# Optimization experiments

Hardware: AMD Instinct MI355X
Metric: run time of the kernel (lower is better)

## Reference

```python
import jax, jax.numpy as jnp
import numpy as np

N = 1024      # params.input_dim (f1 is a square [N, N] similarity matrix)
TOPK = 16     # params.topk
B = 64        # hardcoded batch in the original reshape
W = 2 * N // B  # spatial width after reshape


def setup_inputs() -> dict:
    key = jax.random.key(0)
    k1, k2, k3 = jax.random.split(key, 3)
    f1 = jax.random.normal(k1, (N, N), dtype=jnp.float32)
    # Conv2d(in=N, out=N, kernel=(TOPK, 1)) weights, kaiming-ish scale
    conv_w = jax.random.normal(k2, (N, N, TOPK, 1), dtype=jnp.float32) * 0.01
    conv_b = jax.random.normal(k3, (N,), dtype=jnp.float32) * 0.01
    return {"f1": f1, "conv_w": conv_w, "conv_b": conv_b}


def reference(f1, conv_w, conv_b):
    # i = topk indices along last dim (largest, sorted) -> [N, TOPK]
    _, idx = jax.lax.top_k(f1, TOPK)
    # pos = f1[i]: gather rows of f1 by the topk column indices -> [N, TOPK, N]
    pos = f1[idx]
    # repeat_interleave(TOPK, dim=0).reshape(N, TOPK, -1) == each row tiled TOPK times
    rep = jnp.broadcast_to(f1[:, None, :], (N, TOPK, N))
    # cat on dim=2 -> [N, TOPK, 2N]; reshape to NCHW [B, N, TOPK, W]
    out = jnp.concatenate([rep, pos], axis=2).reshape(B, N, TOPK, W)
    # Conv2d kernel (TOPK, 1), VALID padding collapses H -> 1: [B, N, 1, W]
    y = jax.lax.conv_general_dilated(
        out, conv_w, window_strides=(1, 1), padding='VALID',
        dimension_numbers=('NCHW', 'OIHW', 'NCHW'))
    y = y + conv_b[None, :, None, None]
    return jax.nn.relu(y).reshape(N, -1)  # [N, B*W] = [N, 2N]
```

## Files before the change

### kernel.cpp

```cpp
#include <hip/hip_runtime.h>
#include <stdint.h>


#define NDIM 1024
#define TK   16
#define KPOS 8192
#define KREP 512
#define NCOL 2048

typedef unsigned short u16;
typedef uint32_t u32;
typedef u16   u16x8  __attribute__((ext_vector_type(8)));
typedef __bf16 bf16x8 __attribute__((ext_vector_type(8)));
typedef float  f32x4  __attribute__((ext_vector_type(4)));

__device__ __forceinline__ u16 f2bf(float x) {
    union { float f; unsigned u; } v; v.f = x;
    unsigned r = 0x7FFFu + ((v.u >> 16) & 1u);
    return (u16)((v.u + r) >> 16);
}

__device__ __forceinline__ void load_lds_16B(const u16* g, u16* l) {
    __builtin_amdgcn_global_load_lds(
        (__attribute__((address_space(1))) void*)(uintptr_t)g,
        (__attribute__((address_space(3))) void*)(unsigned)(uintptr_t)l,
        16, 0, 0);
}

#define PREP_TOPK 256
#define PREP_ZERO 512
#define PREP_W    1024
#define PREP_F1T  256

__global__ __launch_bounds__(256) void prep_kernel(const float* __restrict__ f1,
                                                   const float* __restrict__ W,
                                                   int* __restrict__ idx,
                                                   u16* __restrict__ Wb,
                                                   u16* __restrict__ W1b,
                                                   u16* __restrict__ f1t,
                                                   float* __restrict__ out) {
    const int bid = blockIdx.x;
    const int t = threadIdx.x;
    if (bid < PREP_TOPK) {
        const int lane = t & 63;
        const int row  = bid * 4 + (t >> 6);
        float v[16];
        const float* src = f1 + row * NDIM + lane;
        #pragma unroll
        for (int j = 0; j < 16; ++j) v[j] = src[j * 64];
        for (int sel = 0; sel < TK; ++sel) {
            float best = -3.402823466e38f; int bg = 0x7fffffff;
            #pragma unroll
            for (int j = 0; j < 16; ++j)
                if (v[j] > best) { best = v[j]; bg = j * 64 + lane; }
            #pragma unroll
            for (int s = 1; s < 64; s <<= 1) {
                float ov = __shfl_xor(best, s);
                int   og = __shfl_xor(bg, s);
                if (ov > best || (ov == best && og < bg)) { best = ov; bg = og; }
            }
            if (lane == sel) idx[row * TK + sel] = bg;
            #pragma unroll
            for (int j = 0; j < 16; ++j)
                if (bg == j * 64 + lane) v[j] = -3.402823466e38f;
        }
    } else if (bid < PREP_TOPK + PREP_ZERO) {
        const int zb = bid - PREP_TOPK;
        f32x4 z = {0.f, 0.f, 0.f, 0.f};
        float* p = out + (size_t)zb * 4096 + t * 16;
        #pragma unroll
        for (int j = 0; j < 4; ++j) *(f32x4*)(p + j * 4) = z;
    } else if (bid < PREP_TOPK + PREP_ZERO + PREP_W) {
        const int o = bid - PREP_TOPK - PREP_ZERO;
        const float* wrow = W + (size_t)o * 16384;
        u16* wbrow = Wb + (size_t)o * KPOS;
        #pragma unroll
        for (int j = 0; j < 4; ++j) {
            const int v = j * 2048 + t * 8;
            const int u = ((v >> 5) << 6) + 32 + (v & 31);
            float4 a = *(const float4*)(wrow + u);
            float4 b = *(const float4*)(wrow + u + 4);
            u16x8 ov;
            ov[0] = f2bf(a.x); ov[1] = f2bf(a.y); ov[2] = f2bf(a.z); ov[3] = f2bf(a.w);
            ov[4] = f2bf(b.x); ov[5] = f2bf(b.y); ov[6] = f2bf(b.z); ov[7] = f2bf(b.w);
            *(u16x8*)(wbrow + v) = ov;
        }
        #pragma unroll
        for (int h = 0; h < 2; ++h) {
            const int kr = h * 256 + t;
            const int nl = kr >> 5, e = kr & 31;
            const float* base = wrow + nl * 1024 + e;
            float s = 0.f;
            #pragma unroll
            for (int tt = 0; tt < 16; ++tt) s += base[tt * 64];
            W1b[o * KREP + kr] = f2bf(s);
        }
    } else {
        const int gb = bid - PREP_TOPK - PREP_ZERO - PREP_W;
        const int unit = t >> 5;
        const int w = t & 31;
        const int rq = gb * 8 + unit;
        const int row = rq >> 1, q = rq & 1;
        const float* src = f1 + row * NDIM + q * 512;
        const int swp = ((w >> 2) & 1) * 8;
        u16 tmp[16];
        #pragma unroll
        for (int kh = 0; kh < 16; ++kh)
            tmp[kh ^ swp] = f2bf(src[kh * 32 + w]);
        u16* dst = f1t + ((size_t)row * 2 + q) * 512 + w * 16;
        *(u16x8*)(dst)     = *(u16x8*)(tmp);
        *(u16x8*)(dst + 8) = *(u16x8*)(tmp + 8);
    }
}

#define BM 128
#define BN 128
#define BK 64
#define KITERS 34

__global__ __launch_bounds__(256, 2) void gemm_kernel(const u16* __restrict__ Ap,
                                                      const u16* __restrict__ A1,
                                                      const u16* __restrict__ f1t,
                                                      const int* __restrict__ idx,
                                                      float* __restrict__ out) {
    __shared__ __align__(16) u16 As[2][BM * BK];
    __shared__ __align__(16) u16 Bs[2][16 * 512];
    __shared__ int idxL[256];
    const int f = blockIdx.x;
    const int m = f & 7;
    const int g = f >> 3;
    const int n = g & 15;
    const int z = g >> 4;
    const int t    = threadIdx.x;
    const int lane = t & 63;
    const int wave = t >> 6;
    const int wm   = (wave >> 1) * 64;
    const int wn   = (wave & 1) * 64;
    const int quad = lane >> 4;
    const int l16  = lane & 15;
    const int sw   = l16 & 7;
    const int o0 = m * BM;
    const int n0 = n * BN;
    const int nb0 = n * 4;
    const int kb = z * 2048;
    const int nl0 = z * 4;

    {
        const int bl = t >> 6, nlz = (t >> 4) & 3, tt = t & 15;
        idxL[t] = idx[((nb0 + bl) * 16 + nl0 + nlz) * TK + tt];
    }

    f32x4 acc[4][4] = {};

    const int rA = t >> 3;
    const int c8 = t & 7;
    const int csw = (c8 ^ (rA & 7)) * 8;
    const u16* gApos = Ap + (size_t)(o0 + rA) * KPOS + kb + csw;
    const u16* gArep = A1 + (size_t)(o0 + rA) * KREP + z * 128 + csw;
    const int ipbp = kb >> 4;
    const int ipbr = z * 8;

    auto stage = [&](int it, int nb) {
        u16* lA = As[nb] + t * 8;
        int rows[4], qp;
        if (it < 32) {
            const int k0 = it * BK;
            #pragma unroll
            for (int c = 0; c < 4; ++c)
                load_lds_16B(gApos + (size_t)(c * 32) * KPOS + k0, lA + c * 2048);
            const int ip = ipbp + it * 4 + wave;
            qp = ip & 1;
            const int nlz = (ip >> 5) & 3, tt = (ip >> 1) & 15;
            #pragma unroll
            for (int bl = 0; bl < 4; ++bl)
                rows[bl] = idxL[bl * 64 + nlz * 16 + tt];
        } else {
            const int k0 = (it - 32) * BK;
            #pragma unroll
            for (int c = 0; c < 4; ++c)
                load_lds_16B(gArep + (size_t)(c * 32) * KREP + k0, lA + c * 2048);
            const int ip = ipbr + (it - 32) * 4 + wave;
            qp = ip & 1;
            const int nlr = ip >> 1;
            #pragma unroll
            for (int bl = 0; bl < 4; ++bl)
                rows[bl] = (nb0 + bl) * 16 + nlr;
        }
        #pragma unroll
        for (int bl = 0; bl < 4; ++bl)
            load_lds_16B(f1t + ((size_t)rows[bl] * 2 + qp) * 512 + lane * 8,
                         Bs[nb] + (wave * 4 + bl) * 512);
    };

    __syncthreads();
    stage(0, 0);
    __syncthreads();

    for (int it = 0; it < KITERS; ++it) {
        const int cur = it & 1;
        if (it + 1 < KITERS) stage(it + 1, 1 - cur);

        #pragma unroll
        for (int ks = 0; ks < 2; ++ks) {
            bf16x8 af[4], bfr[4];
            #pragma unroll
            for (int mt = 0; mt < 4; ++mt) {
                u16x8 bits = *(const u16x8*)(As[cur] + (wm + mt * 16 + l16) * BK
                                                + (((ks * 4 + quad) ^ sw) * 8));
                af[mt] = __builtin_bit_cast(bf16x8, bits);
            }
            const int ci2 = ks * 2 + (quad >> 1);
            const int qh  = quad & 1;
            #pragma unroll
            for (int nt = 0; nt < 4; ++nt) {
                const int nn = wn + nt * 16 + l16;
                const int blocf = nn >> 5, w = nn & 31;
                u16x8 bits = *(const u16x8*)(Bs[cur] + (ci2 * 4 + blocf) * 512 + w * 16
                                                + ((qh ^ ((w >> 2) & 1)) * 8));
                bfr[nt] = __builtin_bit_cast(bf16x8, bits);
            }
            #pragma unroll
            for (int mt = 0; mt < 4; ++mt)
                #pragma unroll
                for (int nt = 0; nt < 4; ++nt)
                    acc[mt][nt] = __builtin_amdgcn_mfma_f32_16x16x32_bf16(
                        af[mt], bfr[nt], acc[mt][nt], 0, 0, 0);
        }
        __syncthreads();
    }

    #pragma unroll
    for (int nt = 0; nt < 4; ++nt) {
        const int nn = n0 + wn + nt * 16 + l16;
        const int bb = nn >> 5, w = nn & 31;
        #pragma unroll
        for (int mt = 0; mt < 4; ++mt) {
            #pragma unroll
            for (int r = 0; r < 4; ++r) {
                const int o = o0 + wm + mt * 16 + quad * 4 + r;
                unsafeAtomicAdd(out + (size_t)(bb * 16 + (o >> 6)) * 2048
                                    + (o & 63) * 32 + w,
                                acc[mt][nt][r]);
            }
        }
    }
}

__global__ __launch_bounds__(256) void finalize_kernel(float* __restrict__ out,
                                                       const float* __restrict__ bias) {
    const int tid = blockIdx.x * 256 + threadIdx.x;
    const int f = tid * 4;
    const int o = ((f >> 11) & 15) * 64 + ((f & 2047) >> 5);
    const float bv = bias[o];
    float4 x = *(float4*)(out + f);
    x.x = fmaxf(x.x + bv, 0.f);
    x.y = fmaxf(x.y + bv, 0.f);
    x.z = fmaxf(x.z + bv, 0.f);
    x.w = fmaxf(x.w + bv, 0.f);
    *(float4*)(out + f) = x;
}

extern "C" void kernel_launch(void* const* d_in, const int* in_sizes, int n_in,
                              void* d_out, int out_size, void* d_ws, size_t ws_size,
                              hipStream_t stream) {
    const float* f1   = (const float*)d_in[0];
    const float* Wc   = (const float*)d_in[1];
    const float* bias = (const float*)d_in[2];
    float* out = (float*)d_out;

    int* idx = (int*)d_ws;
    u16* Wb  = (u16*)((char*)d_ws + 65536);
    u16* W1b = (u16*)((char*)d_ws + 16842752);
    u16* f1t = (u16*)((char*)d_ws + 17891328);

    prep_kernel<<<PREP_TOPK + PREP_ZERO + PREP_W + PREP_F1T,
                  256, 0, stream>>>(f1, Wc, idx, Wb, W1b, f1t, out);
    gemm_kernel<<<512, 256, 0, stream>>>(Wb, W1b, f1t, idx, out);
    finalize_kernel<<<(NDIM * NCOL) / (4 * 256), 256, 0, stream>>>(out, bias);
}
```

Before: 164.1 us.

## Halve GEMM K-tile and double split-K blocks for higher occupancy

Cuts the GEMM K step from 64 to 32 and doubles the split-K factor, so 1024 blocks are launched instead of 512 and each block covers half the K range. LDS use per block is halved and launch bounds now request 4 blocks per CU, which is meant to raise occupancy and spread work more evenly across CUs. The staging index math, LDS swizzle and idx preload are reworked to match. In exchange, twice as many float atomic adds go to the output, and each iteration has fewer MFMAs per barrier, which may add synchronisation overhead.

```diff
diff --git a/kernel.cpp b/kernel.cpp
--- a/kernel.cpp
+++ b/kernel.cpp
@@ -115,17 +115,17 @@
 
 #define BM 128
 #define BN 128
-#define BK 64
+#define BK 32
 #define KITERS 34
 
-__global__ __launch_bounds__(256, 2) void gemm_kernel(const u16* __restrict__ Ap,
+__global__ __launch_bounds__(256, 4) void gemm_kernel(const u16* __restrict__ Ap,
                                                       const u16* __restrict__ A1,
                                                       const u16* __restrict__ f1t,
                                                       const int* __restrict__ idx,
                                                       float* __restrict__ out) {
     __shared__ __align__(16) u16 As[2][BM * BK];
-    __shared__ __align__(16) u16 Bs[2][16 * 512];
-    __shared__ int idxL[256];
+    __shared__ __align__(16) u16 Bs[2][8 * 512];
+    __shared__ int idxL[128];
     const int f = blockIdx.x;
     const int m = f & 7;
     const int g = f >> 3;
@@ -138,58 +138,49 @@
     const int wn   = (wave & 1) * 64;
     const int quad = lane >> 4;
     const int l16  = lane & 15;
-    const int sw   = l16 & 7;
+    const int key16 = (l16 >> 1) & 3;
     const int o0 = m * BM;
     const int n0 = n * BN;
     const int nb0 = n * 4;
-    const int kb = z * 2048;
-    const int nl0 = z * 4;
-
-    {
-        const int bl = t >> 6, nlz = (t >> 4) & 3, tt = t & 15;
-        idxL[t] = idx[((nb0 + bl) * 16 + nl0 + nlz) * TK + tt];
+    const int kb = z * 1024;
+
+    if (t < 128) {
+        const int bl = t >> 5, nlz = (t >> 4) & 1, tt = t & 15;
+        idxL[t] = idx[((nb0 + bl) * 16 + z * 2 + nlz) * TK + tt];
     }
 
     f32x4 acc[4][4] = {};
 
-    const int rA = t >> 3;
-    const int c8 = t & 7;
-    const int csw = (c8 ^ (rA & 7)) * 8;
+    const int rA = t >> 2;
+    const int csw = ((t & 3) ^ ((t >> 3) & 3)) * 8;
     const u16* gApos = Ap + (size_t)(o0 + rA) * KPOS + kb + csw;
-    const u16* gArep = A1 + (size_t)(o0 + rA) * KREP + z * 128 + csw;
-    const int ipbp = kb >> 4;
-    const int ipbr = z * 8;
+    const u16* gArep = A1 + (size_t)(o0 + rA) * KREP + z * 64 + csw;
+    const int ci = wave >> 1;
+    const int blh = (wave & 1) * 2;
 
     auto stage = [&](int it, int nb) {
         u16* lA = As[nb] + t * 8;
-        int rows[4], qp;
+        int rows[2];
         if (it < 32) {
             const int k0 = it * BK;
-            #pragma unroll
-            for (int c = 0; c < 4; ++c)
-                load_lds_16B(gApos + (size_t)(c * 32) * KPOS + k0, lA + c * 2048);
-            const int ip = ipbp + it * 4 + wave;
-            qp = ip & 1;
-            const int nlz = (ip >> 5) & 3, tt = (ip >> 1) & 15;
-            #pragma unroll
-            for (int bl = 0; bl < 4; ++bl)
-                rows[bl] = idxL[bl * 64 + nlz * 16 + tt];
+            load_lds_16B(gApos + k0, lA);
+            load_lds_16B(gApos + (size_t)64 * KPOS + k0, lA + 2048);
+            const int tt = it & 15, nlz = it >> 4;
+            #pragma unroll
+            for (int jb = 0; jb < 2; ++jb)
+                rows[jb] = idxL[(blh + jb) * 32 + nlz * 16 + tt];
         } else {
             const int k0 = (it - 32) * BK;
-            #pragma unroll
-            for (int c = 0; c < 4; ++c)
-                load_lds_16B(gArep + (size_t)(c * 32) * KREP + k0, lA + c * 2048);
-            const int ip = ipbr + (it - 32) * 4 + wave;
-            qp = ip & 1;
-            const int nlr = ip >> 1;
-            #pragma unroll
-            for (int bl = 0; bl < 4; ++bl)
-                rows[bl] = (nb0 + bl) * 16 + nlr;
-        }
-        #pragma unroll
-        for (int bl = 0; bl < 4; ++bl)
-            load_lds_16B(f1t + ((size_t)rows[bl] * 2 + qp) * 512 + lane * 8,
-                         Bs[nb] + (wave * 4 + bl) * 512);
+            load_lds_16B(gArep + k0, lA);
+            load_lds_16B(gArep + (size_t)64 * KREP + k0, lA + 2048);
+            #pragma unroll
+            for (int jb = 0; jb < 2; ++jb)
+                rows[jb] = (nb0 + blh + jb) * 16 + z * 2 + (it - 32);
+        }
+        #pragma unroll
+        for (int jb = 0; jb < 2; ++jb)
+            load_lds_16B(f1t + ((size_t)rows[jb] * 2 + ci) * 512 + lane * 8,
+                         Bs[nb] + (ci * 4 + blh + jb) * 512);
     };
 
     __syncthreads();
@@ -200,32 +191,30 @@
         const int cur = it & 1;
         if (it + 1 < KITERS) stage(it + 1, 1 - cur);
 
-        #pragma unroll
-        for (int ks = 0; ks < 2; ++ks) {
-            bf16x8 af[4], bfr[4];
-            #pragma unroll
-            for (int mt = 0; mt < 4; ++mt) {
-                u16x8 bits = *(const u16x8*)(As[cur] + (wm + mt * 16 + l16) * BK
-                                                + (((ks * 4 + quad) ^ sw) * 8));
-                af[mt] = __builtin_bit_cast(bf16x8, bits);
-            }
-            const int ci2 = ks * 2 + (quad >> 1);
-            const int qh  = quad & 1;
-            #pragma unroll
-            for (int nt = 0; nt < 4; ++nt) {
-                const int nn = wn + nt * 16 + l16;
-                const int blocf = nn >> 5, w = nn & 31;
-                u16x8 bits = *(const u16x8*)(Bs[cur] + (ci2 * 4 + blocf) * 512 + w * 16
-                                                + ((qh ^ ((w >> 2) & 1)) * 8));
-                bfr[nt] = __builtin_bit_cast(bf16x8, bits);
-            }
-            #pragma unroll
-            for (int mt = 0; mt < 4; ++mt)
-                #pragma unroll
-                for (int nt = 0; nt < 4; ++nt)
-                    acc[mt][nt] = __builtin_amdgcn_mfma_f32_16x16x32_bf16(
-                        af[mt], bfr[nt], acc[mt][nt], 0, 0, 0);
-        }
+        bf16x8 af[4], bfr[4];
+        #pragma unroll
+        for (int mt = 0; mt < 4; ++mt) {
+            u16x8 bits = *(const u16x8*)(As[cur] + (wm + mt * 16 + l16) * BK
+                                            + ((quad ^ key16) * 8));
+            af[mt] = __builtin_bit_cast(bf16x8, bits);
+        }
+        const int ci2 = quad >> 1;
+        const int qh  = quad & 1;
+        #pragma unroll
+        for (int nt = 0; nt < 4; ++nt) {
+            const int nn = wn + nt * 16 + l16;
+            const int blocf = nn >> 5, w = nn & 31;
+            u16x8 bits = *(const u16x8*)(Bs[cur] + (ci2 * 4 + blocf) * 512 + w * 16
+                                            + ((qh ^ ((w >> 2) & 1)) * 8));
+            bfr[nt] = __builtin_bit_cast(bf16x8, bits);
+        }
+        #pragma unroll
+        for (int mt = 0; mt < 4; ++mt)
+            #pragma unroll
+            for (int nt = 0; nt < 4; ++nt)
+                acc[mt][nt] = __builtin_amdgcn_mfma_f32_16x16x32_bf16(
+                    af[mt], bfr[nt], acc[mt][nt], 0, 0, 0);
+
         __syncthreads();
     }
 
@@ -275,6 +264,6 @@
 
     prep_kernel<<<PREP_TOPK + PREP_ZERO + PREP_W + PREP_F1T,
                   256, 0, stream>>>(f1, Wc, idx, Wb, W1b, f1t, out);
-    gemm_kernel<<<512, 256, 0, stream>>>(Wb, W1b, f1t, idx, out);
+    gemm_kernel<<<1024, 256, 0, stream>>>(Wb, W1b, f1t, idx, out);
     finalize_kernel<<<(NDIM * NCOL) / (4 * 256), 256, 0, stream>>>(out, bias);
 }
```

Result: slower. 188.1 us (+14.6%).

## Load B fragments directly from global into registers, bypassing LDS staging

Applied to the files above, without the earlier changes.

Removes the LDS staging buffer for the gathered B operand. Each wave now reads its MFMA B fragments straight from global memory into registers, double-buffered across a loop unrolled by two. This cuts LDS traffic and shared memory use, which may allow higher occupancy. In exchange it adds register pressure and issues uncoalesced 16-byte global loads whose latency the compute must hide, and data that other waves previously shared through LDS is now loaded redundantly.

```diff
diff --git a/kernel.cpp b/kernel.cpp
--- a/kernel.cpp
+++ b/kernel.cpp
@@ -124,7 +124,6 @@
                                                       const int* __restrict__ idx,
                                                       float* __restrict__ out) {
     __shared__ __align__(16) u16 As[2][BM * BK];
-    __shared__ __align__(16) u16 Bs[2][16 * 512];
     __shared__ int idxL[256];
     const int f = blockIdx.x;
     const int m = f & 7;
@@ -139,6 +138,9 @@
     const int quad = lane >> 4;
     const int l16  = lane & 15;
     const int sw   = l16 & 7;
+    const int qh   = quad & 1;
+    const int cihalf = quad >> 1;
+    const int bl0  = wn >> 5;
     const int o0 = m * BM;
     const int n0 = n * BN;
     const int nb0 = n * 4;
@@ -160,72 +162,98 @@
     const int ipbp = kb >> 4;
     const int ipbr = z * 8;
 
-    auto stage = [&](int it, int nb) {
+    int bofs[4];
+    #pragma unroll
+    for (int nt = 0; nt < 4; ++nt) {
+        const int nn = wn + nt * 16 + l16;
+        const int w = nn & 31;
+        bofs[nt] = w * 16 + ((qh ^ ((w >> 2) & 1)) * 8);
+    }
+
+    auto stageA = [&](int it, int nb) {
         u16* lA = As[nb] + t * 8;
-        int rows[4], qp;
         if (it < 32) {
             const int k0 = it * BK;
             #pragma unroll
             for (int c = 0; c < 4; ++c)
                 load_lds_16B(gApos + (size_t)(c * 32) * KPOS + k0, lA + c * 2048);
-            const int ip = ipbp + it * 4 + wave;
-            qp = ip & 1;
-            const int nlz = (ip >> 5) & 3, tt = (ip >> 1) & 15;
-            #pragma unroll
-            for (int bl = 0; bl < 4; ++bl)
-                rows[bl] = idxL[bl * 64 + nlz * 16 + tt];
         } else {
             const int k0 = (it - 32) * BK;
             #pragma unroll
             for (int c = 0; c < 4; ++c)
                 load_lds_16B(gArep + (size_t)(c * 32) * KREP + k0, lA + c * 2048);
-            const int ip = ipbr + (it - 32) * 4 + wave;
-            qp = ip & 1;
-            const int nlr = ip >> 1;
-            #pragma unroll
-            for (int bl = 0; bl < 4; ++bl)
-                rows[bl] = (nb0 + bl) * 16 + nlr;
-        }
-        #pragma unroll
-        for (int bl = 0; bl < 4; ++bl)
-            load_lds_16B(f1t + ((size_t)rows[bl] * 2 + qp) * 512 + lane * 8,
-                         Bs[nb] + (wave * 4 + bl) * 512);
+        }
     };
 
-    __syncthreads();
-    stage(0, 0);
-    __syncthreads();
-
-    for (int it = 0; it < KITERS; ++it) {
-        const int cur = it & 1;
-        if (it + 1 < KITERS) stage(it + 1, 1 - cur);
-
+    auto loadB = [&](int it, u16x8* dst) {
+        int offs[2][2];
+        if (it < 32) {
+            #pragma unroll
+            for (int ks = 0; ks < 2; ++ks) {
+                const int ip = ipbp + it * 4 + ks * 2 + cihalf;
+                const int qp = ip & 1, nlz = (ip >> 5) & 3, tt = (ip >> 1) & 15;
+                #pragma unroll
+                for (int j = 0; j < 2; ++j) {
+                    const int row = idxL[(bl0 + j) * 64 + nlz * 16 + tt];
+                    offs[ks][j] = (row * 2 + qp) * 512;
+                }
+            }
+        } else {
+            #pragma unroll
+            for (int ks = 0; ks < 2; ++ks) {
+                const int ip = ipbr + (it - 32) * 4 + ks * 2 + cihalf;
+                const int qp = ip & 1, nlr = ip >> 1;
+                #pragma unroll
+                for (int j = 0; j < 2; ++j)
+                    offs[ks][j] = (((nb0 + bl0 + j) * 16 + nlr) * 2 + qp) * 512;
+            }
+        }
+        #pragma unroll
+        for (int ks = 0; ks < 2; ++ks)
+            #pragma unroll
+            for (int nt = 0; nt < 4; ++nt)
+                dst[ks * 4 + nt] =
+                    *(const u16x8*)(f1t + offs[ks][nt >> 1] + bofs[nt]);
+    };
+
+    auto compute = [&](const u16* AsX, const u16x8* b) {
         #pragma unroll
         for (int ks = 0; ks < 2; ++ks) {
-            bf16x8 af[4], bfr[4];
+            bf16x8 af[4];
             #pragma unroll
             for (int mt = 0; mt < 4; ++mt) {
-                u16x8 bits = *(const u16x8*)(As[cur] + (wm + mt * 16 + l16) * BK
+                u16x8 bits = *(const u16x8*)(AsX + (wm + mt * 16 + l16) * BK
                                                 + (((ks * 4 + quad) ^ sw) * 8));
                 af[mt] = __builtin_bit_cast(bf16x8, bits);
-            }
-            const int ci2 = ks * 2 + (quad >> 1);
-            const int qh  = quad & 1;
-            #pragma unroll
-            for (int nt = 0; nt < 4; ++nt) {
-                const int nn = wn + nt * 16 + l16;
-                const int blocf = nn >> 5, w = nn & 31;
-                u16x8 bits = *(const u16x8*)(Bs[cur] + (ci2 * 4 + blocf) * 512 + w * 16
-                                                + ((qh ^ ((w >> 2) & 1)) * 8));
-                bfr[nt] = __builtin_bit_cast(bf16x8, bits);
             }
             #pragma unroll
             for (int mt = 0; mt < 4; ++mt)
                 #pragma unroll
                 for (int nt = 0; nt < 4; ++nt)
                     acc[mt][nt] = __builtin_amdgcn_mfma_f32_16x16x32_bf16(
-                        af[mt], bfr[nt], acc[mt][nt], 0, 0, 0);
-        }
+                        af[mt], __builtin_bit_cast(bf16x8, b[ks * 4 + nt]),
+                        acc[mt][nt], 0, 0, 0);
+        }
+    };
+
+    u16x8 b0[8], b1[8];
+
+    __syncthreads();
+    stageA(0, 0);
+    loadB(0, b0);
+    __syncthreads();
+
+    for (int it = 0; it < KITERS; it += 2) {
+        stageA(it + 1, 1);
+        loadB(it + 1, b1);
+        compute(As[0], b0);
+        __syncthreads();
+
+        if (it + 2 < KITERS) {
+            stageA(it + 2, 0);
+            loadB(it + 2, b0);
+        }
+        compute(As[1], b1);
         __syncthreads();
     }
 
```

Result: slower. 170.9 us (+4.1%).

## Fuse prep, GEMM and finalize into one persistent kernel with grid barriers

Applied to the files above, without the earlier changes.

Merges the prep, GEMM and bias/ReLU finalize kernels into one 512-block kernel. Each block handles several virtual prep blocks and finalize chunks, and a software grid barrier with atomic counters separates the phases. Zeroing the output moves to hipMemsetAsync. The aim is to cut kernel launch gaps and tail idling between stages. It relies on all 512 blocks being co-resident, and the counter-reset scheme could race if a block is still spinning when another resets its counter.

```diff
diff --git a/kernel.cpp b/kernel.cpp
--- a/kernel.cpp
+++ b/kernel.cpp
@@ -7,6 +7,7 @@
 #define KPOS 8192
 #define KREP 512
 #define NCOL 2048
+#define NBLK 512
 
 typedef unsigned short u16;
 typedef uint32_t u32;
@@ -14,6 +15,8 @@
 typedef __bf16 bf16x8 __attribute__((ext_vector_type(8)));
 typedef float  f32x4  __attribute__((ext_vector_type(4)));
 
+__device__ int g_ctr1, g_ctr2;
+
 __device__ __forceinline__ u16 f2bf(float x) {
     union { float f; unsigned u; } v; v.f = x;
     unsigned r = 0x7FFFu + ((v.u >> 16) & 1u);
@@ -27,23 +30,36 @@
         16, 0, 0);
 }
 
+__device__ __forceinline__ void global_barrier(int* arrive, int* resetOther) {
+    __threadfence();
+    __syncthreads();
+    if (threadIdx.x == 0) {
+        __hip_atomic_store(resetOther, 0, __ATOMIC_RELAXED,
+                           __HIP_MEMORY_SCOPE_AGENT);
+        __hip_atomic_fetch_add(arrive, 1, __ATOMIC_ACQ_REL,
+                               __HIP_MEMORY_SCOPE_AGENT);
+        while (__hip_atomic_load(arrive, __ATOMIC_ACQUIRE,
+                                 __HIP_MEMORY_SCOPE_AGENT) < NBLK)
+            __builtin_amdgcn_s_sleep(2);
+        __threadfence();
+    }
+    __syncthreads();
+}
+
 #define PREP_TOPK 256
-#define PREP_ZERO 512
 #define PREP_W    1024
 #define PREP_F1T  256
 
-__global__ __launch_bounds__(256) void prep_kernel(const float* __restrict__ f1,
-                                                   const float* __restrict__ W,
-                                                   int* __restrict__ idx,
-                                                   u16* __restrict__ Wb,
-                                                   u16* __restrict__ W1b,
-                                                   u16* __restrict__ f1t,
-                                                   float* __restrict__ out) {
-    const int bid = blockIdx.x;
-    const int t = threadIdx.x;
-    if (bid < PREP_TOPK) {
+__device__ __forceinline__ void prep_virtual(int vb, int t,
+                                             const float* __restrict__ f1,
+                                             const float* __restrict__ W,
+                                             int* __restrict__ idx,
+                                             u16* __restrict__ Wb,
+                                             u16* __restrict__ W1b,
+                                             u16* __restrict__ f1t) {
+    if (vb < PREP_TOPK) {
         const int lane = t & 63;
-        const int row  = bid * 4 + (t >> 6);
+        const int row  = vb * 4 + (t >> 6);
         float v[16];
         const float* src = f1 + row * NDIM + lane;
         #pragma unroll
@@ -64,14 +80,8 @@
             for (int j = 0; j < 16; ++j)
                 if (bg == j * 64 + lane) v[j] = -3.402823466e38f;
         }
-    } else if (bid < PREP_TOPK + PREP_ZERO) {
-        const int zb = bid - PREP_TOPK;
-        f32x4 z = {0.f, 0.f, 0.f, 0.f};
-        float* p = out + (size_t)zb * 4096 + t * 16;
-        #pragma unroll
-        for (int j = 0; j < 4; ++j) *(f32x4*)(p + j * 4) = z;
-    } else if (bid < PREP_TOPK + PREP_ZERO + PREP_W) {
-        const int o = bid - PREP_TOPK - PREP_ZERO;
+    } else if (vb < PREP_TOPK + PREP_W) {
+        const int o = vb - PREP_TOPK;
         const float* wrow = W + (size_t)o * 16384;
         u16* wbrow = Wb + (size_t)o * KPOS;
         #pragma unroll
@@ -96,7 +106,7 @@
             W1b[o * KREP + kr] = f2bf(s);
         }
     } else {
-        const int gb = bid - PREP_TOPK - PREP_ZERO - PREP_W;
+        const int gb = vb - PREP_TOPK - PREP_W;
         const int unit = t >> 5;
         const int w = t & 31;
         const int rq = gb * 8 + unit;
@@ -118,146 +128,162 @@
 #define BK 64
 #define KITERS 34
 
-__global__ __launch_bounds__(256, 2) void gemm_kernel(const u16* __restrict__ Ap,
-                                                      const u16* __restrict__ A1,
-                                                      const u16* __restrict__ f1t,
-                                                      const int* __restrict__ idx,
-                                                      float* __restrict__ out) {
+__global__ __launch_bounds__(256, 2) void fused_kernel(const float* __restrict__ f1,
+                                                       const float* __restrict__ W,
+                                                       const float* __restrict__ bias,
+                                                       int* __restrict__ idx,
+                                                       u16* __restrict__ Wb,
+                                                       u16* __restrict__ W1b,
+                                                       u16* __restrict__ f1t,
+                                                       float* __restrict__ out) {
     __shared__ __align__(16) u16 As[2][BM * BK];
     __shared__ __align__(16) u16 Bs[2][16 * 512];
     __shared__ int idxL[256];
+
     const int f = blockIdx.x;
-    const int m = f & 7;
-    const int g = f >> 3;
-    const int n = g & 15;
-    const int z = g >> 4;
-    const int t    = threadIdx.x;
-    const int lane = t & 63;
-    const int wave = t >> 6;
-    const int wm   = (wave >> 1) * 64;
-    const int wn   = (wave & 1) * 64;
-    const int quad = lane >> 4;
-    const int l16  = lane & 15;
-    const int sw   = l16 & 7;
-    const int o0 = m * BM;
-    const int n0 = n * BN;
-    const int nb0 = n * 4;
-    const int kb = z * 2048;
-    const int nl0 = z * 4;
+    const int t = threadIdx.x;
+
+    #pragma unroll 1
+    for (int i = 0; i < 3; ++i)
+        prep_virtual(f + NBLK * i, t, f1, W, idx, Wb, W1b, f1t);
+
+    global_barrier(&g_ctr1, &g_ctr2);
 
     {
-        const int bl = t >> 6, nlz = (t >> 4) & 3, tt = t & 15;
-        idxL[t] = idx[((nb0 + bl) * 16 + nl0 + nlz) * TK + tt];
+        const int m = f & 7;
+        const int g = f >> 3;
+        const int n = g & 15;
+        const int z = g >> 4;
+        const int lane = t & 63;
+        const int wave = t >> 6;
+        const int wm   = (wave >> 1) * 64;
+        const int wn   = (wave & 1) * 64;
+        const int quad = lane >> 4;
+        const int l16  = lane & 15;
+        const int sw   = l16 & 7;
+        const int o0 = m * BM;
+        const int n0 = n * BN;
+        const int nb0 = n * 4;
+        const int kb = z * 2048;
+        const int nl0 = z * 4;
+
+        {
+            const int bl = t >> 6, nlz = (t >> 4) & 3, tt = t & 15;
+            idxL[t] = idx[((nb0 + bl) * 16 + nl0 + nlz) * TK + tt];
+        }
+
+        f32x4 acc[4][4] = {};
+
+        const int rA = t >> 3;
+        const int c8 = t & 7;
+        const int csw = (c8 ^ (rA & 7)) * 8;
+        const u16* gApos = Wb + (size_t)(o0 + rA) * KPOS + kb + csw;
+        const u16* gArep = W1b + (size_t)(o0 + rA) * KREP + z * 128 + csw;
+        const int ipbp = kb >> 4;
+        const int ipbr = z * 8;
+
+        auto stage = [&](int it, int nb) {
+            u16* lA = As[nb] + t * 8;
+            int rows[4], qp;
+            if (it < 32) {
+                const int k0 = it * BK;
+                #pragma unroll
+                for (int c = 0; c < 4; ++c)
+                    load_lds_16B(gApos + (size_t)(c * 32) * KPOS + k0, lA + c * 2048);
+                const int ip = ipbp + it * 4 + wave;
+                qp = ip & 1;
+                const int nlz = (ip >> 5) & 3, tt = (ip >> 1) & 15;
+                #pragma unroll
+                for (int bl = 0; bl < 4; ++bl)
+                    rows[bl] = idxL[bl * 64 + nlz * 16 + tt];
+            } else {
+                const int k0 = (it - 32) * BK;
+                #pragma unroll
+                for (int c = 0; c < 4; ++c)
+                    load_lds_16B(gArep + (size_t)(c * 32) * KREP + k0, lA + c * 2048);
+                const int ip = ipbr + (it - 32) * 4 + wave;
+                qp = ip & 1;
+                const int nlr = ip >> 1;
+                #pragma unroll
+                for (int bl = 0; bl < 4; ++bl)
+                    rows[bl] = (nb0 + bl) * 16 + nlr;
+            }
+            #pragma unroll
+            for (int bl = 0; bl < 4; ++bl)
+                load_lds_16B(f1t + ((size_t)rows[bl] * 2 + qp) * 512 + lane * 8,
+                             Bs[nb] + (wave * 4 + bl) * 512);
+        };
+
+        __syncthreads();
+        stage(0, 0);
+        __syncthreads();
+
+        for (int it = 0; it < KITERS; ++it) {
+            const int cur = it & 1;
+            if (it + 1 < KITERS) stage(it + 1, 1 - cur);
+
+            #pragma unroll
+            for (int ks = 0; ks < 2; ++ks) {
+                bf16x8 af[4], bfr[4];
+                #pragma unroll
+                for (int mt = 0; mt < 4; ++mt) {
+                    u16x8 bits = *(const u16x8*)(As[cur] + (wm + mt * 16 + l16) * BK
+                                                    + (((ks * 4 + quad) ^ sw) * 8));
+                    af[mt] = __builtin_bit_cast(bf16x8, bits);
+                }
+                const int ci2 = ks * 2 + (quad >> 1);
+                const int qh  = quad & 1;
+                #pragma unroll
+                for (int nt = 0; nt < 4; ++nt) {
+                    const int nn = wn + nt * 16 + l16;
+                    const int blocf = nn >> 5, w = nn & 31;
+                    u16x8 bits = *(const u16x8*)(Bs[cur] + (ci2 * 4 + blocf) * 512 + w * 16
+                                                    + ((qh ^ ((w >> 2) & 1)) * 8));
+                    bfr[nt] = __builtin_bit_cast(bf16x8, bits);
+                }
+                #pragma unroll
+                for (int mt = 0; mt < 4; ++mt)
+                    #pragma unroll
+                    for (int nt = 0; nt < 4; ++nt)
+                        acc[mt][nt] = __builtin_amdgcn_mfma_f32_16x16x32_bf16(
+                            af[mt], bfr[nt], acc[mt][nt], 0, 0, 0);
+            }
+            __syncthreads();
+        }
+
+        #pragma unroll
+        for (int nt = 0; nt < 4; ++nt) {
+            const int nn = n0 + wn + nt * 16 + l16;
+            const int bb = nn >> 5, w = nn & 31;
+            #pragma unroll
+            for (int mt = 0; mt < 4; ++mt) {
+                #pragma unroll
+                for (int r = 0; r < 4; ++r) {
+                    const int o = o0 + wm + mt * 16 + quad * 4 + r;
+                    unsafeAtomicAdd(out + (size_t)(bb * 16 + (o >> 6)) * 2048
+                                        + (o & 63) * 32 + w,
+                                    acc[mt][nt][r]);
+                }
+            }
+        }
     }
 
-    f32x4 acc[4][4] = {};
-
-    const int rA = t >> 3;
-    const int c8 = t & 7;
-    const int csw = (c8 ^ (rA & 7)) * 8;
-    const u16* gApos = Ap + (size_t)(o0 + rA) * KPOS + kb + csw;
-    const u16* gArep = A1 + (size_t)(o0 + rA) * KREP + z * 128 + csw;
-    const int ipbp = kb >> 4;
-    const int ipbr = z * 8;
-
-    auto stage = [&](int it, int nb) {
-        u16* lA = As[nb] + t * 8;
-        int rows[4], qp;
-        if (it < 32) {
-            const int k0 = it * BK;
-            #pragma unroll
-            for (int c = 0; c < 4; ++c)
-                load_lds_16B(gApos + (size_t)(c * 32) * KPOS + k0, lA + c * 2048);
-            const int ip = ipbp + it * 4 + wave;
-            qp = ip & 1;
-            const int nlz = (ip >> 5) & 3, tt = (ip >> 1) & 15;
-            #pragma unroll
-            for (int bl = 0; bl < 4; ++bl)
-                rows[bl] = idxL[bl * 64 + nlz * 16 + tt];
-        } else {
-            const int k0 = (it - 32) * BK;
-            #pragma unroll
-            for (int c = 0; c < 4; ++c)
-                load_lds_16B(gArep + (size_t)(c * 32) * KREP + k0, lA + c * 2048);
-            const int ip = ipbr + (it - 32) * 4 + wave;
-            qp = ip & 1;
-            const int nlr = ip >> 1;
-            #pragma unroll
-            for (int bl = 0; bl < 4; ++bl)
-                rows[bl] = (nb0 + bl) * 16 + nlr;
-        }
-        #pragma unroll
-        for (int bl = 0; bl < 4; ++bl)
-            load_lds_16B(f1t + ((size_t)rows[bl] * 2 + qp) * 512 + lane * 8,
-                         Bs[nb] + (wave * 4 + bl) * 512);
-    };
-
-    __syncthreads();
-    stage(0, 0);
-    __syncthreads();
-
-    for (int it = 0; it < KITERS; ++it) {
-        const int cur = it & 1;
-        if (it + 1 < KITERS) stage(it + 1, 1 - cur);
-
-        #pragma unroll
-        for (int ks = 0; ks < 2; ++ks) {
-            bf16x8 af[4], bfr[4];
-            #pragma unroll
-            for (int mt = 0; mt < 4; ++mt) {
-                u16x8 bits = *(const u16x8*)(As[cur] + (wm + mt * 16 + l16) * BK
-                                                + (((ks * 4 + quad) ^ sw) * 8));
-                af[mt] = __builtin_bit_cast(bf16x8, bits);
-            }
-            const int ci2 = ks * 2 + (quad >> 1);
-            const int qh  = quad & 1;
-            #pragma unroll
-            for (int nt = 0; nt < 4; ++nt) {
-                const int nn = wn + nt * 16 + l16;
-                const int blocf = nn >> 5, w = nn & 31;
-                u16x8 bits = *(const u16x8*)(Bs[cur] + (ci2 * 4 + blocf) * 512 + w * 16
-                                                + ((qh ^ ((w >> 2) & 1)) * 8));
-                bfr[nt] = __builtin_bit_cast(bf16x8, bits);
-            }
-            #pragma unroll
-            for (int mt = 0; mt < 4; ++mt)
-                #pragma unroll
-                for (int nt = 0; nt < 4; ++nt)
-                    acc[mt][nt] = __builtin_amdgcn_mfma_f32_16x16x32_bf16(
-                        af[mt], bfr[nt], acc[mt][nt], 0, 0, 0);
-        }
-        __syncthreads();
+    global_barrier(&g_ctr2, &g_ctr1);
+
+    #pragma unroll 1
+    for (int i = 0; i < 4; ++i) {
+        const int vb = f + NBLK * i;
+        const int tid = vb * 256 + t;
+        const int p = tid * 4;
+        const int o = ((p >> 11) & 15) * 64 + ((p & 2047) >> 5);
+        const float bv = bias[o];
+        float4 x = *(float4*)(out + p);
+        x.x = fmaxf(x.x + bv, 0.f);
+        x.y = fmaxf(x.y + bv, 0.f);
+        x.z = fmaxf(x.z + bv, 0.f);
+        x.w = fmaxf(x.w + bv, 0.f);
+        *(float4*)(out + p) = x;
     }
-
-    #pragma unroll
-    for (int nt = 0; nt < 4; ++nt) {
-        const int nn = n0 + wn + nt * 16 + l16;
-        const int bb = nn >> 5, w = nn & 31;
-        #pragma unroll
-        for (int mt = 0; mt < 4; ++mt) {
-            #pragma unroll
-            for (int r = 0; r < 4; ++r) {
-                const int o = o0 + wm + mt * 16 + quad * 4 + r;
-                unsafeAtomicAdd(out + (size_t)(bb * 16 + (o >> 6)) * 2048
-                                    + (o & 63) * 32 + w,
-                                acc[mt][nt][r]);
-            }
-        }
-    }
-}
-
-__global__ __launch_bounds__(256) void finalize_kernel(float* __restrict__ out,
-                                                       const float* __restrict__ bias) {
-    const int tid = blockIdx.x * 256 + threadIdx.x;
-    const int f = tid * 4;
-    const int o = ((f >> 11) & 15) * 64 + ((f & 2047) >> 5);
-    const float bv = bias[o];
-    float4 x = *(float4*)(out + f);
-    x.x = fmaxf(x.x + bv, 0.f);
-    x.y = fmaxf(x.y + bv, 0.f);
-    x.z = fmaxf(x.z + bv, 0.f);
-    x.w = fmaxf(x.w + bv, 0.f);
-    *(float4*)(out + f) = x;
 }
 
 extern "C" void kernel_launch(void* const* d_in, const int* in_sizes, int n_in,
@@ -273,8 +299,6 @@
     u16* W1b = (u16*)((char*)d_ws + 16842752);
     u16* f1t = (u16*)((char*)d_ws + 17891328);
 
-    prep_kernel<<<PREP_TOPK + PREP_ZERO + PREP_W + PREP_F1T,
-                  256, 0, stream>>>(f1, Wc, idx, Wb, W1b, f1t, out);
-    gemm_kernel<<<512, 256, 0, stream>>>(Wb, W1b, f1t, idx, out);
-    finalize_kernel<<<(NDIM * NCOL) / (4 * 256), 256, 0, stream>>>(out, bias);
-}
+    hipMemsetAsync(out, 0, (size_t)NDIM * NCOL * sizeof(float), stream);
+    fused_kernel<<<NBLK, 256, 0, stream>>>(f1, Wc, bias, idx, Wb, W1b, f1t, out);
+}
```

Measured after the change: 424.4 us. 159% more time.
